# Kernel optimization log

Hardware: AMD Instinct MI355X
Metric: run time of the kernel (lower is better)

Reference implementation:

```python
import jax, jax.numpy as jnp
import numpy as np

N = 50000
E = 800000
IN_C = 128
OUT_C = 64
NEG_SLOPE = 0.2


def setup_inputs() -> dict:
    key = jax.random.key(0)
    k1, k2, k3, k4, k5 = jax.random.split(key, 5)
    x = jax.random.normal(k1, (N, IN_C), dtype=jnp.float32)
    edge_index = jax.random.randint(k2, (2, E), 0, N, dtype=jnp.int64)
    # GATv2Conv params (heads=1): lin_l (source), lin_r (target), att, bias
    sc_in = 1.0 / np.sqrt(IN_C)
    sc_out = 1.0 / np.sqrt(OUT_C)
    W_l = jax.random.normal(k3, (IN_C, OUT_C), dtype=jnp.float32) * sc_in
    W_r = jax.random.normal(k4, (IN_C, OUT_C), dtype=jnp.float32) * sc_in
    att = jax.random.normal(k5, (OUT_C,), dtype=jnp.float32) * sc_out
    bias = jnp.zeros((OUT_C,), dtype=jnp.float32)
    return {"x": x, "edge_index": edge_index, "W_l": W_l, "W_r": W_r,
            "att": att, "bias": bias}


def _gatv2(x, edge_index, W_l, W_r, att, bias):
    n = x.shape[0]
    # add self loops (PyG default add_self_loops=True)
    loop = jnp.arange(n, dtype=edge_index.dtype)
    src = jnp.concatenate([edge_index[0], loop])
    dst = jnpp_concat = jnp.concatenate([edge_index[1], loop])
    x_l = x @ W_l  # source transform [N, C]
    x_r = x @ W_r  # target transform [N, C]
    x_j = x_l[src]                      # [E+N, C] gathered source msgs
    e = jax.nn.leaky_relu(x_j + x_r[dst], NEG_SLOPE)
    logit = e @ att                     # [E+N]
    # segment softmax over edges grouped by destination node
    m = jax.ops.segment_max(logit, dst, num_segments=n)
    m = jnp.where(jnp.isfinite(m), m, 0.0)
    a = jnp.exp(logit - m[dst])
    denom = jax.ops.segment_sum(a, dst, num_segments=n)
    alpha = a / (denom[dst] + 1e-16)
    out = jax.ops.segment_sum(x_j * alpha[:, None], dst, num_segments=n)
    return out + bias


def reference(x, edge_index, W_l, W_r, att, bias):
    # dropout(p=0.6) is identity at inference
    h = jax.nn.elu(_gatv2(x, edge_index, W_l, W_r, att, bias))
    return jax.nn.log_softmax(h, axis=-1)
```

## Files before the change

### kernel.cpp

```cpp
#include <hip/hip_runtime.h>

#define N_NODES 50000
#define N_EDGES 800000
#define IN_C    128
#define OUT_C   64
#define NEG_SLOPE 0.2f

#define CAP     48

#define NB      196
#define NB_PAD  256
#define C_B     5120
#define EPB     4096
#define NP1     ((N_EDGES + EPB - 1) / EPB)

#define G_GEMM  ((N_NODES + 63) / 64)

typedef __bf16 bf16_8 __attribute__((ext_vector_type(8)));
typedef float  f32x4  __attribute__((ext_vector_type(4)));

__device__ __forceinline__ unsigned f2bf(float f) {
    unsigned u = __float_as_uint(f);
    return (u + 0x7fffu + ((u >> 16) & 1u)) >> 16;
}

__global__ __launch_bounds__(256) void k_prep(
    const float* __restrict__ Wl, const float* __restrict__ Wr,
    unsigned short* __restrict__ wtg, int* __restrict__ bcnt)
{
    int i = blockIdx.x * 256 + threadIdx.x;
    int k = i >> 6, cm = i & 63;
    if (k < 128) {
        wtg[(size_t)cm * 128 + k]        = (unsigned short)f2bf(Wl[(size_t)k * 64 + cm]);
        wtg[(size_t)(64 + cm) * 128 + k] = (unsigned short)f2bf(Wr[(size_t)k * 64 + cm]);
    }
    if (i < NB_PAD) bcnt[i] = 0;
}

#define XPAD 136
__global__ __launch_bounds__(256) void k_gemm_p1(
    const float* __restrict__ x, const unsigned short* __restrict__ wtg,
    const float* __restrict__ att, const int* __restrict__ ei,
    int* __restrict__ bcnt, unsigned* __restrict__ arena,
    unsigned short* __restrict__ xlb, unsigned short* __restrict__ xrb,
    float* __restrict__ qtil)
{
    __shared__ __align__(16) char smem[20480];

    const int tid = threadIdx.x;

    if (blockIdx.x >= G_GEMM) {
        unsigned* sorted = (unsigned*)smem;
        int* bc     = (int*)(smem + 16384);
        int* bstart = (int*)(smem + 16384 + 1024);
        int* gbase  = (int*)(smem + 16384 + 2048);
        int* bofs   = (int*)(smem + 16384 + 3072);

        int bid = blockIdx.x - G_GEMM;
        int e0 = bid * EPB;
        int nE = N_EDGES - e0; if (nE > EPB) nE = EPB;

        unsigned pk[16]; int bk[16];
#pragma unroll
        for (int jj = 0; jj < 4; ++jj) {
            int rel = jj * 1024 + tid * 4;
            if (rel + 3 < nE) {
                int4 d4 = *(const int4*)(ei + N_EDGES + e0 + rel);
                int4 s4 = *(const int4*)(ei + e0 + rel);
                int d[4] = {d4.x, d4.y, d4.z, d4.w};
                int s[4] = {s4.x, s4.y, s4.z, s4.w};
#pragma unroll
                for (int k2 = 0; k2 < 4; ++k2) {
                    pk[jj*4+k2] = ((unsigned)d[k2] << 16) | (unsigned)s[k2];
                    bk[jj*4+k2] = d[k2] >> 8;
                }
            } else {
#pragma unroll
                for (int k2 = 0; k2 < 4; ++k2) {
                    int e = rel + k2;
                    if (e < nE) {
                        int d = ei[N_EDGES + e0 + e], s = ei[e0 + e];
                        pk[jj*4+k2] = ((unsigned)d << 16) | (unsigned)s;
                        bk[jj*4+k2] = d >> 8;
                    } else bk[jj*4+k2] = -1;
                }
            }
        }

        bc[tid] = 0;
        __syncthreads();
#pragma unroll
        for (int i = 0; i < 16; ++i)
            if (bk[i] >= 0) atomicAdd(&bc[bk[i]], 1);
        __syncthreads();
        if (tid < 64) {
            int c0 = bc[tid*4], c1 = bc[tid*4+1], c2 = bc[tid*4+2], c3 = bc[tid*4+3];
            int t0 = c0, t1 = t0 + c1, t2 = t1 + c2, t3 = t2 + c3;
            int incl = t3;
#pragma unroll
            for (int o = 1; o < 64; o <<= 1) {
                int v = __shfl_up(incl, o);
                if (tid >= o) incl += v;
            }
            int ex = incl - t3;
            bstart[tid*4]   = ex;
            bstart[tid*4+1] = ex + t0;
            bstart[tid*4+2] = ex + t1;
            bstart[tid*4+3] = ex + t2;
        }
        __syncthreads();
        {
            int c = bc[tid];
            bofs[tid] = bstart[tid];
            if (c > 0) gbase[tid] = atomicAdd(&bcnt[tid], c);
        }
        __syncthreads();
#pragma unroll
        for (int i = 0; i < 16; ++i)
            if (bk[i] >= 0) {
                int p = atomicAdd(&bofs[bk[i]], 1);
                sorted[p] = pk[i];
            }
        __syncthreads();
        for (int p = tid; p < nE; p += 256) {
            unsigned v = sorted[p];
            int b = v >> 24;
            int g = gbase[b] + (p - bstart[b]);
            if (g < C_B) arena[(size_t)b * C_B + g] = v;
        }
        return;
    }

    unsigned short* xs = (unsigned short*)smem;
    const int nbase = blockIdx.x * 64;

    const float4* x4 = (const float4*)x;
    for (int i = tid; i < 2048; i += 256) {
        int row = i >> 5, qq = i & 31;
        int node = nbase + row;
        float4 v = make_float4(0.f, 0.f, 0.f, 0.f);
        if (node < N_NODES) v = x4[(size_t)node * 32 + qq];
        uint2 p;
        p.x = f2bf(v.x) | (f2bf(v.y) << 16);
        p.y = f2bf(v.z) | (f2bf(v.w) << 16);
        *(uint2*)&xs[row * XPAD + qq * 4] = p;
    }
    __syncthreads();

    const int lane = tid & 63, wave = tid >> 6;
    const int m = lane & 15, quad = lane >> 4;

    bf16_8 af[4];
#pragma unroll
    for (int kt = 0; kt < 4; ++kt)
        af[kt] = *(const bf16_8*)&xs[(wave * 16 + m) * XPAD + kt * 32 + quad * 8];

    f32x4 accs[4];
#pragma unroll
    for (int t = 0; t < 4; ++t) {
        f32x4 acc = {0.f, 0.f, 0.f, 0.f};
#pragma unroll
        for (int kt = 0; kt < 4; ++kt) {
            bf16_8 bfr = *(const bf16_8*)&wtg[(size_t)(t * 16 + m) * 128 + kt * 32 + quad * 8];
            acc = __builtin_amdgcn_mfma_f32_16x16x32_bf16(af[kt], bfr, acc, 0, 0, 0);
        }
        accs[t] = acc;
#pragma unroll
        for (int r = 0; r < 4; ++r) {
            int node = nbase + wave * 16 + quad * 4 + r;
            if (node < N_NODES)
                xlb[(size_t)node * 64 + t * 16 + m] = (unsigned short)f2bf(acc[r]);
        }
    }
    {
        float am[4];
#pragma unroll
        for (int t = 0; t < 4; ++t) am[t] = 0.6f * att[t * 16 + m];
        float part[4];
#pragma unroll
        for (int r = 0; r < 4; ++r) {
            part[r] = am[0] * accs[0][r];
#pragma unroll
            for (int t = 1; t < 4; ++t) part[r] = fmaf(am[t], accs[t][r], part[r]);
        }
#pragma unroll
        for (int o = 1; o <= 8; o <<= 1)
#pragma unroll
            for (int r = 0; r < 4; ++r) part[r] += __shfl_xor(part[r], o);
        if (m == 0) {
#pragma unroll
            for (int r = 0; r < 4; ++r) {
                int node = nbase + wave * 16 + quad * 4 + r;
                if (node < N_NODES) qtil[node] = part[r];
            }
        }
    }
#pragma unroll
    for (int t = 4; t < 8; ++t) {
        f32x4 acc = {0.f, 0.f, 0.f, 0.f};
#pragma unroll
        for (int kt = 0; kt < 4; ++kt) {
            bf16_8 bfr = *(const bf16_8*)&wtg[(size_t)(t * 16 + m) * 128 + kt * 32 + quad * 8];
            acc = __builtin_amdgcn_mfma_f32_16x16x32_bf16(af[kt], bfr, acc, 0, 0, 0);
        }
        int col = t * 16 + m - 64;
#pragma unroll
        for (int r = 0; r < 4; ++r) {
            int node = nbase + wave * 16 + quad * 4 + r;
            if (node < N_NODES)
                xrb[(size_t)node * 64 + col] = (unsigned short)f2bf(acc[r]);
        }
    }
}

__global__ __launch_bounds__(256) void k_csr(
    const unsigned* __restrict__ arena, const int* __restrict__ bcnt,
    int* __restrict__ cnt, unsigned short* __restrict__ csr_src)
{
    __shared__ __align__(16) unsigned short lcsr[256 * CAP];
    __shared__ int lcnt[256];
    const int b = blockIdx.x, tid = threadIdx.x;
    const int n0 = b << 8;
    int nloc = N_NODES - n0; if (nloc > 256) nloc = 256;

    lcnt[tid] = 0;
    __syncthreads();

    int ne = bcnt[b]; if (ne > C_B) ne = C_B;
    const unsigned* ap = arena + (size_t)b * C_B;
    for (int p = tid; p < ne; p += 256) {
        unsigned v = ap[p];
        int dl  = (v >> 16) & 255;
        int pos = atomicAdd(&lcnt[dl], 1);
        if (pos < CAP) lcsr[dl * CAP + pos] = (unsigned short)(v & 0xffffu);
    }
    __syncthreads();

    if (tid < nloc) {
        int pos = lcnt[tid];
        if (pos < CAP) lcsr[tid * CAP + pos] = (unsigned short)(n0 + tid);
        cnt[n0 + tid] = pos + 1;
    }
    __syncthreads();

    const uint4* ls = (const uint4*)lcsr;
    uint4* gd = (uint4*)(csr_src + (size_t)n0 * CAP);
    int nv = nloc * 6;
    for (int i = tid; i < nv; i += 256) gd[i] = ls[i];
}

__global__ __launch_bounds__(256) void k_fused(
    const int* __restrict__ cnt, const unsigned short* __restrict__ csr_src,
    const unsigned short* __restrict__ xlb, const unsigned short* __restrict__ xrb,
    const float* __restrict__ qtil, const float* __restrict__ att,
    const float* __restrict__ bias, float* __restrict__ out)
{
    int wid  = (blockIdx.x * 256 + threadIdx.x) >> 6;
    if (wid >= N_NODES) return;
    unsigned lane = threadIdx.x & 63;
    unsigned g = lane >> 3;
    unsigned q = lane & 7;

    const uint4* xl4 = (const uint4*)xlb;
    const unsigned short* cs = csr_src + (unsigned)wid * CAP;

    uint4 XR = ((const uint4*)xrb)[(unsigned)wid * 8 + q];
    float xrv[8];
    xrv[0] = __uint_as_float(XR.x << 16); xrv[1] = __uint_as_float(XR.x & 0xffff0000u);
    xrv[2] = __uint_as_float(XR.y << 16); xrv[3] = __uint_as_float(XR.y & 0xffff0000u);
    xrv[4] = __uint_as_float(XR.z << 16); xrv[5] = __uint_as_float(XR.z & 0xffff0000u);
    xrv[6] = __uint_as_float(XR.w << 16); xrv[7] = __uint_as_float(XR.w & 0xffff0000u);

    const float4* atp = (const float4*)(att + q * 8);
    float4 ata = atp[0], atb = atp[1];
    float atv[8] = {ata.x, ata.y, ata.z, ata.w, atb.x, atb.y, atb.z, atb.w};
#pragma unroll
    for (int j = 0; j < 8; ++j) atv[j] *= 0.4f;

    int deg = cnt[wid];
    if (deg > CAP) deg = CAP;
    int iters = (deg + 7) >> 3;

    float s = 0.f;
    float acc[8] = {0.f, 0.f, 0.f, 0.f, 0.f, 0.f, 0.f, 0.f};

    int e = (int)g;
    bool va = e < deg;
    unsigned sA = va ? (unsigned)cs[e] : (unsigned)wid;
    uint4 A = xl4[(sA << 3) + q];
    float QA = qtil[sA];
    e += 8;
    bool vb = e < deg;
    unsigned sB = vb ? (unsigned)cs[e] : (unsigned)wid;
    uint4 B = xl4[(sB << 3) + q];
    float QB = qtil[sB];

    for (int it = 0; it < iters; ++it) {
        uint4 C = A; float QC = QA; bool vc = va;
        A = B; QA = QB; va = vb;
        e += 8;
        vb = e < deg;
        unsigned sN = vb ? (unsigned)cs[e] : (unsigned)wid;
        B = xl4[(sN << 3) + q];
        QB = qtil[sN];

        float c[8];
        c[0] = __uint_as_float(C.x << 16);
        c[1] = __uint_as_float(C.x & 0xffff0000u);
        c[2] = __uint_as_float(C.y << 16);
        c[3] = __uint_as_float(C.y & 0xffff0000u);
        c[4] = __uint_as_float(C.z << 16);
        c[5] = __uint_as_float(C.z & 0xffff0000u);
        c[6] = __uint_as_float(C.w << 16);
        c[7] = __uint_as_float(C.w & 0xffff0000u);

        float r = 0.f;
#pragma unroll
        for (int j = 0; j < 8; ++j) {
            float t = c[j] + xrv[j];
            r = fmaf(atv[j], fabsf(t), r);
        }
        r += __shfl_xor(r, 1);
        r += __shfl_xor(r, 2);
        r += __shfl_xor(r, 4);

        float w = vc ? __expf(QC + r) : 0.f;
        s += w;
#pragma unroll
        for (int j = 0; j < 8; ++j) acc[j] = fmaf(w, c[j], acc[j]);
    }

#pragma unroll
    for (int o = 8; o <= 32; o <<= 1) {
        s += __shfl_xor(s, o);
#pragma unroll
        for (int j = 0; j < 8; ++j) acc[j] += __shfl_xor(acc[j], o);
    }

    float inv = 1.f / (s + 1e-16f);
    const float4* bp = (const float4*)(bias + q * 8);
    float4 ba = bp[0], bb = bp[1];
    float bv[8] = {ba.x, ba.y, ba.z, ba.w, bb.x, bb.y, bb.z, bb.w};
    float h[8];
    float mx = -INFINITY;
#pragma unroll
    for (int j = 0; j < 8; ++j) {
        float hh = fmaf(acc[j], inv, bv[j]);
        hh = (hh > 0.f) ? hh : (__expf(hh) - 1.f);
        h[j] = hh;
        mx = fmaxf(mx, hh);
    }
#pragma unroll
    for (int o = 1; o <= 4; o <<= 1) mx = fmaxf(mx, __shfl_xor(mx, o));
    float ex = 0.f;
#pragma unroll
    for (int j = 0; j < 8; ++j) ex += __expf(h[j] - mx);
#pragma unroll
    for (int o = 1; o <= 4; o <<= 1) ex += __shfl_xor(ex, o);
    float lse = mx + __logf(ex);

    if (g == 0) {
        float4* op = (float4*)(out + (unsigned)wid * 64 + q * 8);
        op[0] = make_float4(h[0] - lse, h[1] - lse, h[2] - lse, h[3] - lse);
        op[1] = make_float4(h[4] - lse, h[5] - lse, h[6] - lse, h[7] - lse);
    }
}

extern "C" void kernel_launch(void* const* d_in, const int* in_sizes, int n_in,
                              void* d_out, int out_size, void* d_ws, size_t ws_size,
                              hipStream_t stream)
{
    const float* x    = (const float*)d_in[0];
    const int*   ei   = (const int*)  d_in[1];
    const float* Wl   = (const float*)d_in[2];
    const float* Wr   = (const float*)d_in[3];
    const float* att  = (const float*)d_in[4];
    const float* bias = (const float*)d_in[5];
    float* out = (float*)d_out;

    char* w = (char*)d_ws;
    unsigned short* xlb = (unsigned short*)w; w += (size_t)N_NODES * 64 * 2;
    unsigned short* xrb = (unsigned short*)w; w += (size_t)N_NODES * 64 * 2;
    unsigned short* csr_src = (unsigned short*)w; w += (size_t)N_NODES * CAP * 2;
    int*   cnt     = (int*)w;    w += (size_t)N_NODES * 4;
    float* qtil    = (float*)w;  w += (size_t)N_NODES * 4;
    unsigned short* wtg = (unsigned short*)w; w += (size_t)128 * 128 * 2;
    unsigned* arena = (unsigned*)w; w += (size_t)NB * C_B * 4;
    int* bcnt = (int*)w; w += (size_t)NB_PAD * 4;

    k_prep   <<<32,                         256, 0, stream>>>(Wl, Wr, wtg, bcnt);
    k_gemm_p1<<<G_GEMM + NP1,               256, 0, stream>>>(
        x, wtg, att, ei, bcnt, arena, xlb, xrb, qtil);
    k_csr    <<<NB,                         256, 0, stream>>>(arena, bcnt, cnt, csr_src);
    k_fused  <<<(N_NODES * 64 + 255) / 256, 256, 0, stream>>>(
        cnt, csr_src, xlb, xrb, qtil, att, bias, out);
}
```

Before: 145.7 us.

## Fuse GEMM, bucketing, CSR build and aggregation into a persistent megakernel

Replaces the three launches (GEMM+bucketing, CSR build, fused aggregation) with a single persistent kernel of 1024 blocks that uses global atomic counters as grid barriers. Bucketing blocks spin on a partial barrier and then build the CSR for their own bucket. All blocks meet at a full grid barrier before running the per-node aggregation loop with a grid-stride over waves. The aim is to remove launch gaps and tail effects between stages. The cost is spin-wait overhead and a dependence on all 1024 blocks being co-resident, which is checked once through an occupancy query, with a fallback to the old path.

```diff
diff --git a/kernel.cpp b/kernel.cpp
--- a/kernel.cpp
+++ b/kernel.cpp
@@ -13,8 +13,9 @@
 #define C_B     5120
 #define EPB     4096
 #define NP1     ((N_EDGES + EPB - 1) / EPB)
-
 #define G_GEMM  ((N_NODES + 63) / 64)
+
+#define GRID_MEGA 1024
 
 typedef __bf16 bf16_8 __attribute__((ext_vector_type(8)));
 typedef float  f32x4  __attribute__((ext_vector_type(4)));
@@ -22,6 +23,25 @@
 __device__ __forceinline__ unsigned f2bf(float f) {
     unsigned u = __float_as_uint(f);
     return (u + 0x7fffu + ((u >> 16) & 1u)) >> 16;
+}
+
+__device__ __forceinline__ void wait_ge(int* ctr, int target) {
+    int it = 0;
+    while (__hip_atomic_load(ctr, __ATOMIC_ACQUIRE, __HIP_MEMORY_SCOPE_AGENT) < target) {
+        __builtin_amdgcn_s_sleep(2);
+        if (++it > (1 << 26)) break;
+    }
+}
+
+__device__ __forceinline__ void grid_barrier(int* ctr, int nblk) {
+    __syncthreads();
+    if (threadIdx.x == 0) {
+        __threadfence();
+        __hip_atomic_fetch_add(ctr, 1, __ATOMIC_ACQ_REL, __HIP_MEMORY_SCOPE_AGENT);
+        wait_ge(ctr, nblk);
+        __threadfence();
+    }
+    __syncthreads();
 }
 
 __global__ __launch_bounds__(256) void k_prep(
@@ -34,10 +54,343 @@
         wtg[(size_t)cm * 128 + k]        = (unsigned short)f2bf(Wl[(size_t)k * 64 + cm]);
         wtg[(size_t)(64 + cm) * 128 + k] = (unsigned short)f2bf(Wr[(size_t)k * 64 + cm]);
     }
-    if (i < NB_PAD) bcnt[i] = 0;
+    if (i < NB_PAD + 8) bcnt[i] = 0;
 }
 
 #define XPAD 136
+
+__global__ __launch_bounds__(256, 4) void k_mega(
+    const float* __restrict__ x, const unsigned short* __restrict__ wtg,
+    const float* __restrict__ att, const int* __restrict__ ei,
+    int* __restrict__ bcnt, unsigned* __restrict__ arena,
+    unsigned short* __restrict__ xlb, unsigned short* __restrict__ xrb,
+    float* __restrict__ qtil, int* __restrict__ cnt,
+    unsigned short* __restrict__ csr_src, const float* __restrict__ bias,
+    float* __restrict__ out)
+{
+    __shared__ __align__(16) char smem[25600];
+    const int tid = threadIdx.x;
+    const int b = (int)blockIdx.x;
+    const int nblk = (int)gridDim.x;
+    int* p1done = bcnt + NB_PAD;
+    int* fullbar = bcnt + NB_PAD + 1;
+
+    if (b < NP1) {
+        unsigned* sorted = (unsigned*)smem;
+        int* bc     = (int*)(smem + 16384);
+        int* bstart = (int*)(smem + 16384 + 1024);
+        int* gbase  = (int*)(smem + 16384 + 2048);
+        int* bofs   = (int*)(smem + 16384 + 3072);
+
+        int e0 = b * EPB;
+        int nE = N_EDGES - e0; if (nE > EPB) nE = EPB;
+
+        unsigned pk[16]; int bk[16];
+#pragma unroll
+        for (int jj = 0; jj < 4; ++jj) {
+            int rel = jj * 1024 + tid * 4;
+            if (rel + 3 < nE) {
+                int4 d4 = *(const int4*)(ei + N_EDGES + e0 + rel);
+                int4 s4 = *(const int4*)(ei + e0 + rel);
+                int d[4] = {d4.x, d4.y, d4.z, d4.w};
+                int s[4] = {s4.x, s4.y, s4.z, s4.w};
+#pragma unroll
+                for (int k2 = 0; k2 < 4; ++k2) {
+                    pk[jj*4+k2] = ((unsigned)d[k2] << 16) | (unsigned)s[k2];
+                    bk[jj*4+k2] = d[k2] >> 8;
+                }
+            } else {
+#pragma unroll
+                for (int k2 = 0; k2 < 4; ++k2) {
+                    int e = rel + k2;
+                    if (e < nE) {
+                        int d = ei[N_EDGES + e0 + e], s = ei[e0 + e];
+                        pk[jj*4+k2] = ((unsigned)d << 16) | (unsigned)s;
+                        bk[jj*4+k2] = d >> 8;
+                    } else bk[jj*4+k2] = -1;
+                }
+            }
+        }
+
+        bc[tid] = 0;
+        __syncthreads();
+#pragma unroll
+        for (int i = 0; i < 16; ++i)
+            if (bk[i] >= 0) atomicAdd(&bc[bk[i]], 1);
+        __syncthreads();
+        if (tid < 64) {
+            int c0 = bc[tid*4], c1 = bc[tid*4+1], c2 = bc[tid*4+2], c3 = bc[tid*4+3];
+            int t0 = c0, t1 = t0 + c1, t2 = t1 + c2, t3 = t2 + c3;
+            int incl = t3;
+#pragma unroll
+            for (int o = 1; o < 64; o <<= 1) {
+                int v = __shfl_up(incl, o);
+                if (tid >= o) incl += v;
+            }
+            int ex = incl - t3;
+            bstart[tid*4]   = ex;
+            bstart[tid*4+1] = ex + t0;
+            bstart[tid*4+2] = ex + t1;
+            bstart[tid*4+3] = ex + t2;
+        }
+        __syncthreads();
+        {
+            int c = bc[tid];
+            bofs[tid] = bstart[tid];
+            if (c > 0) gbase[tid] = atomicAdd(&bcnt[tid], c);
+        }
+        __syncthreads();
+#pragma unroll
+        for (int i = 0; i < 16; ++i)
+            if (bk[i] >= 0) {
+                int p = atomicAdd(&bofs[bk[i]], 1);
+                sorted[p] = pk[i];
+            }
+        __syncthreads();
+        for (int p = tid; p < nE; p += 256) {
+            unsigned v = sorted[p];
+            int b2 = v >> 24;
+            int gg = gbase[b2] + (p - bstart[b2]);
+            if (gg < C_B) arena[(size_t)b2 * C_B + gg] = v;
+        }
+
+        __syncthreads();
+        if (tid == 0) {
+            __threadfence();
+            __hip_atomic_fetch_add(p1done, 1, __ATOMIC_ACQ_REL, __HIP_MEMORY_SCOPE_AGENT);
+            wait_ge(p1done, NP1);
+            __threadfence();
+        }
+        __syncthreads();
+
+        unsigned short* lcsr = (unsigned short*)smem;
+        int* lcnt = (int*)(smem + 24576);
+        const int n0 = b << 8;
+        int nloc = N_NODES - n0; if (nloc > 256) nloc = 256;
+
+        lcnt[tid] = 0;
+        __syncthreads();
+
+        int ne = bcnt[b]; if (ne > C_B) ne = C_B;
+        const unsigned* ap = arena + (size_t)b * C_B;
+        for (int p = tid; p < ne; p += 256) {
+            unsigned v = ap[p];
+            int dl  = (v >> 16) & 255;
+            int pos = atomicAdd(&lcnt[dl], 1);
+            if (pos < CAP) lcsr[dl * CAP + pos] = (unsigned short)(v & 0xffffu);
+        }
+        __syncthreads();
+
+        if (tid < nloc) {
+            int pos = lcnt[tid];
+            if (pos < CAP) lcsr[tid * CAP + pos] = (unsigned short)(n0 + tid);
+            cnt[n0 + tid] = pos + 1;
+        }
+        __syncthreads();
+
+        const uint4* ls = (const uint4*)lcsr;
+        uint4* gd = (uint4*)(csr_src + (size_t)n0 * CAP);
+        int nv = nloc * 6;
+        for (int i = tid; i < nv; i += 256) gd[i] = ls[i];
+    } else if (b < NP1 + G_GEMM) {
+        unsigned short* xs = (unsigned short*)smem;
+        const int nbase = (b - NP1) * 64;
+
+        const float4* x4 = (const float4*)x;
+        for (int i = tid; i < 2048; i += 256) {
+            int row = i >> 5, qq = i & 31;
+            int node = nbase + row;
+            float4 v = make_float4(0.f, 0.f, 0.f, 0.f);
+            if (node < N_NODES) v = x4[(size_t)node * 32 + qq];
+            uint2 p;
+            p.x = f2bf(v.x) | (f2bf(v.y) << 16);
+            p.y = f2bf(v.z) | (f2bf(v.w) << 16);
+            *(uint2*)&xs[row * XPAD + qq * 4] = p;
+        }
+        __syncthreads();
+
+        const int lane = tid & 63, wave = tid >> 6;
+        const int m = lane & 15, quad = lane >> 4;
+
+        bf16_8 af[4];
+#pragma unroll
+        for (int kt = 0; kt < 4; ++kt)
+            af[kt] = *(const bf16_8*)&xs[(wave * 16 + m) * XPAD + kt * 32 + quad * 8];
+
+        f32x4 accs[4];
+#pragma unroll
+        for (int t = 0; t < 4; ++t) {
+            f32x4 acc = {0.f, 0.f, 0.f, 0.f};
+#pragma unroll
+            for (int kt = 0; kt < 4; ++kt) {
+                bf16_8 bfr = *(const bf16_8*)&wtg[(size_t)(t * 16 + m) * 128 + kt * 32 + quad * 8];
+                acc = __builtin_amdgcn_mfma_f32_16x16x32_bf16(af[kt], bfr, acc, 0, 0, 0);
+            }
+            accs[t] = acc;
+#pragma unroll
+            for (int r = 0; r < 4; ++r) {
+                int node = nbase + wave * 16 + quad * 4 + r;
+                if (node < N_NODES)
+                    xlb[(size_t)node * 64 + t * 16 + m] = (unsigned short)f2bf(acc[r]);
+            }
+        }
+        {
+            float am[4];
+#pragma unroll
+            for (int t = 0; t < 4; ++t) am[t] = 0.6f * att[t * 16 + m];
+            float part[4];
+#pragma unroll
+            for (int r = 0; r < 4; ++r) {
+                part[r] = am[0] * accs[0][r];
+#pragma unroll
+                for (int t = 1; t < 4; ++t) part[r] = fmaf(am[t], accs[t][r], part[r]);
+            }
+#pragma unroll
+            for (int o = 1; o <= 8; o <<= 1)
+#pragma unroll
+                for (int r = 0; r < 4; ++r) part[r] += __shfl_xor(part[r], o);
+            if (m == 0) {
+#pragma unroll
+                for (int r = 0; r < 4; ++r) {
+                    int node = nbase + wave * 16 + quad * 4 + r;
+                    if (node < N_NODES) qtil[node] = part[r];
+                }
+            }
+        }
+#pragma unroll
+        for (int t = 4; t < 8; ++t) {
+            f32x4 acc = {0.f, 0.f, 0.f, 0.f};
+#pragma unroll
+            for (int kt = 0; kt < 4; ++kt) {
+                bf16_8 bfr = *(const bf16_8*)&wtg[(size_t)(t * 16 + m) * 128 + kt * 32 + quad * 8];
+                acc = __builtin_amdgcn_mfma_f32_16x16x32_bf16(af[kt], bfr, acc, 0, 0, 0);
+            }
+            int col = t * 16 + m - 64;
+#pragma unroll
+            for (int r = 0; r < 4; ++r) {
+                int node = nbase + wave * 16 + quad * 4 + r;
+                if (node < N_NODES)
+                    xrb[(size_t)node * 64 + col] = (unsigned short)f2bf(acc[r]);
+            }
+        }
+    }
+
+    grid_barrier(fullbar, nblk);
+
+    const unsigned lane = tid & 63;
+    const unsigned g = lane >> 3;
+    const unsigned q = lane & 7;
+    const int wave = tid >> 6;
+    const int wstride = nblk * 4;
+
+    const uint4* xl4 = (const uint4*)xlb;
+
+    const float4* atp = (const float4*)(att + q * 8);
+    float4 ata = atp[0], atb = atp[1];
+    float atv[8] = {ata.x, ata.y, ata.z, ata.w, atb.x, atb.y, atb.z, atb.w};
+#pragma unroll
+    for (int j = 0; j < 8; ++j) atv[j] *= 0.4f;
+    const float4* bp = (const float4*)(bias + q * 8);
+    float4 ba = bp[0], bb = bp[1];
+    float bv[8] = {ba.x, ba.y, ba.z, ba.w, bb.x, bb.y, bb.z, bb.w};
+
+    for (int wid = b * 4 + wave; wid < N_NODES; wid += wstride) {
+        const unsigned short* cs = csr_src + (unsigned)wid * CAP;
+
+        uint4 XR = ((const uint4*)xrb)[(unsigned)wid * 8 + q];
+        float xrv[8];
+        xrv[0] = __uint_as_float(XR.x << 16); xrv[1] = __uint_as_float(XR.x & 0xffff0000u);
+        xrv[2] = __uint_as_float(XR.y << 16); xrv[3] = __uint_as_float(XR.y & 0xffff0000u);
+        xrv[4] = __uint_as_float(XR.z << 16); xrv[5] = __uint_as_float(XR.z & 0xffff0000u);
+        xrv[6] = __uint_as_float(XR.w << 16); xrv[7] = __uint_as_float(XR.w & 0xffff0000u);
+
+        int deg = cnt[wid];
+        if (deg > CAP) deg = CAP;
+        int iters = (deg + 7) >> 3;
+
+        float s = 0.f;
+        float acc[8] = {0.f, 0.f, 0.f, 0.f, 0.f, 0.f, 0.f, 0.f};
+
+        int e = (int)g;
+        bool va = e < deg;
+        unsigned sA = va ? (unsigned)cs[e] : (unsigned)wid;
+        uint4 A = xl4[(sA << 3) + q];
+        float QA = qtil[sA];
+        e += 8;
+        bool vb = e < deg;
+        unsigned sB = vb ? (unsigned)cs[e] : (unsigned)wid;
+        uint4 B = xl4[(sB << 3) + q];
+        float QB = qtil[sB];
+
+        for (int it = 0; it < iters; ++it) {
+            uint4 C = A; float QC = QA; bool vc = va;
+            A = B; QA = QB; va = vb;
+            e += 8;
+            vb = e < deg;
+            unsigned sN = vb ? (unsigned)cs[e] : (unsigned)wid;
+            B = xl4[(sN << 3) + q];
+            QB = qtil[sN];
+
+            float c[8];
+            c[0] = __uint_as_float(C.x << 16);
+            c[1] = __uint_as_float(C.x & 0xffff0000u);
+            c[2] = __uint_as_float(C.y << 16);
+            c[3] = __uint_as_float(C.y & 0xffff0000u);
+            c[4] = __uint_as_float(C.z << 16);
+            c[5] = __uint_as_float(C.z & 0xffff0000u);
+            c[6] = __uint_as_float(C.w << 16);
+            c[7] = __uint_as_float(C.w & 0xffff0000u);
+
+            float r = 0.f;
+#pragma unroll
+            for (int j = 0; j < 8; ++j) {
+                float t = c[j] + xrv[j];
+                r = fmaf(atv[j], fabsf(t), r);
+            }
+            r += __shfl_xor(r, 1);
+            r += __shfl_xor(r, 2);
+            r += __shfl_xor(r, 4);
+
+            float w = vc ? __expf(QC + r) : 0.f;
+            s += w;
+#pragma unroll
+            for (int j = 0; j < 8; ++j) acc[j] = fmaf(w, c[j], acc[j]);
+        }
+
+#pragma unroll
+        for (int o = 8; o <= 32; o <<= 1) {
+            s += __shfl_xor(s, o);
+#pragma unroll
+            for (int j = 0; j < 8; ++j) acc[j] += __shfl_xor(acc[j], o);
+        }
+
+        float inv = 1.f / (s + 1e-16f);
+        float h[8];
+        float mx = -INFINITY;
+#pragma unroll
+        for (int j = 0; j < 8; ++j) {
+            float hh = fmaf(acc[j], inv, bv[j]);
+            hh = (hh > 0.f) ? hh : (__expf(hh) - 1.f);
+            h[j] = hh;
+            mx = fmaxf(mx, hh);
+        }
+#pragma unroll
+        for (int o = 1; o <= 4; o <<= 1) mx = fmaxf(mx, __shfl_xor(mx, o));
+        float ex = 0.f;
+#pragma unroll
+        for (int j = 0; j < 8; ++j) ex += __expf(h[j] - mx);
+#pragma unroll
+        for (int o = 1; o <= 4; o <<= 1) ex += __shfl_xor(ex, o);
+        float lse = mx + __logf(ex);
+
+        if (g == 0) {
+            float4* op = (float4*)(out + (unsigned)wid * 64 + q * 8);
+            op[0] = make_float4(h[0] - lse, h[1] - lse, h[2] - lse, h[3] - lse);
+            op[1] = make_float4(h[4] - lse, h[5] - lse, h[6] - lse, h[7] - lse);
+        }
+    }
+}
+
 __global__ __launch_bounds__(256) void k_gemm_p1(
     const float* __restrict__ x, const unsigned short* __restrict__ wtg,
     const float* __restrict__ att, const int* __restrict__ ei,
@@ -46,7 +399,6 @@
     float* __restrict__ qtil)
 {
     __shared__ __align__(16) char smem[20480];
-
     const int tid = threadIdx.x;
 
     if (blockIdx.x >= G_GEMM) {
@@ -124,9 +476,9 @@
         __syncthreads();
         for (int p = tid; p < nE; p += 256) {
             unsigned v = sorted[p];
-            int b = v >> 24;
-            int g = gbase[b] + (p - bstart[b]);
-            if (g < C_B) arena[(size_t)b * C_B + g] = v;
+            int b2 = v >> 24;
+            int gg = gbase[b2] + (p - bstart[b2]);
+            if (gg < C_B) arena[(size_t)b2 * C_B + gg] = v;
         }
         return;
     }
@@ -386,12 +738,26 @@
     float* qtil    = (float*)w;  w += (size_t)N_NODES * 4;
     unsigned short* wtg = (unsigned short*)w; w += (size_t)128 * 128 * 2;
     unsigned* arena = (unsigned*)w; w += (size_t)NB * C_B * 4;
-    int* bcnt = (int*)w; w += (size_t)NB_PAD * 4;
-
-    k_prep   <<<32,                         256, 0, stream>>>(Wl, Wr, wtg, bcnt);
-    k_gemm_p1<<<G_GEMM + NP1,               256, 0, stream>>>(
-        x, wtg, att, ei, bcnt, arena, xlb, xrb, qtil);
-    k_csr    <<<NB,                         256, 0, stream>>>(arena, bcnt, cnt, csr_src);
-    k_fused  <<<(N_NODES * 64 + 255) / 256, 256, 0, stream>>>(
-        cnt, csr_src, xlb, xrb, qtil, att, bias, out);
-}
+    int* bcnt = (int*)w; w += (size_t)(NB_PAD + 8) * 4;
+
+    static int mode = -1;
+    if (mode < 0) {
+        int nb = 0;
+        hipError_t err = hipOccupancyMaxActiveBlocksPerMultiprocessor(
+            &nb, reinterpret_cast<const void*>(k_mega), 256, 0);
+        mode = (err == hipSuccess && nb >= 4) ? 1 : 0;
+    }
+
+    k_prep<<<32, 256, 0, stream>>>(Wl, Wr, wtg, bcnt);
+
+    if (mode == 1) {
+        k_mega<<<GRID_MEGA, 256, 0, stream>>>(
+            x, wtg, att, ei, bcnt, arena, xlb, xrb, qtil, cnt, csr_src, bias, out);
+    } else {
+        k_gemm_p1<<<G_GEMM + NP1, 256, 0, stream>>>(
+            x, wtg, att, ei, bcnt, arena, xlb, xrb, qtil);
+        k_csr<<<NB, 256, 0, stream>>>(arena, bcnt, cnt, csr_src);
+        k_fused<<<(N_NODES * 64 + 255) / 256, 256, 0, stream>>>(
+            cnt, csr_src, xlb, xrb, qtil, att, bias, out);
+    }
+}
```

Measured after the change: 143.7 us. Within noise of the previous version (-1.4%).
